# Kernel tuning notes

Measured on AMD Instinct MI355X. Metric: run time of the kernel, lower is better.

Reference implementation:

```python
import jax, jax.numpy as jnp
import numpy as np
import math

B, S, D, H, W = 1, 2048, 512, 8, 64
DK = D // H
NEG = -1e9


def setup_inputs() -> dict:
    rng = jax.random.key(0)
    ks = jax.random.split(rng, 8)
    sc = 0.02
    return {
        "query": jax.random.normal(ks[0], (B, S, D), jnp.float32),
        "key": jax.random.normal(ks[1], (B, S, D), jnp.float32),
        "value": jax.random.normal(ks[2], (B, S, D), jnp.float32),
        "Wq": jax.random.normal(ks[3], (D, D), jnp.float32) * sc,
        "Wk": jax.random.normal(ks[4], (D, D), jnp.float32) * sc,
        "Wv": jax.random.normal(ks[5], (D, D), jnp.float32) * sc,
        "Wo": jax.random.normal(ks[6], (D, D), jnp.float32) * sc,
        "bo": jax.random.normal(ks[7], (D,), jnp.float32) * sc,
    }


def reference(query, key, value, Wq, Wk, Wv, Wo, bo):
    b, s, d = query.shape

    def proj(x, Wm):
        # [B,S,D] -> [B,H,S,DK]
        return (x @ Wm.T).reshape(b, s, H, DK).transpose(0, 2, 1, 3)

    Q = proj(query, Wq)
    K = proj(key, Wk)
    V = proj(value, Wv)

    i = jnp.arange(s)
    rel = jnp.arange(-W, 1)                     # causal band: keys i-W..i
    idx = i[:, None] + rel[None, :]             # [S, W+1]
    valid = idx >= 0
    idxc = jnp.clip(idx, 0, s - 1)

    Kw = K[:, :, idxc, :]                       # [B,H,S,W+1,DK]
    Vw = V[:, :, idxc, :]

    scores = jnp.einsum('bhsd,bhsrd->bhsr', Q, Kw) / math.sqrt(DK)
    decay_bias = 0.1 * jnp.exp(-0.1 * jnp.abs(rel.astype(jnp.float32)))
    scores = jnp.where(valid[None, None], scores + decay_bias, NEG)
    probs = jax.nn.softmax(scores, axis=-1)     # [B,H,S,W+1]

    out = jnp.einsum('bhsr,bhsrd->bhsd', probs, Vw)
    out = out.transpose(0, 2, 1, 3).reshape(b, s, d)
    output = out @ Wo.T + bo

    # attention_weights [B,H,S,2W]: only rows with window_size <= 2W are written
    win = jnp.minimum(s, i + W + 1) - jnp.maximum(0, i - W)   # [S]
    stored = win <= 2 * W
    slot = jnp.arange(2 * W)
    ridx = slot[None, :] + jnp.maximum(W - i, 0)[:, None]     # [S,2W] slot->band index
    vmask = (ridx <= W) & (slot[None, :] < win[:, None]) & stored[:, None]
    gath = jnp.take_along_axis(probs, jnp.clip(ridx, 0, W)[None, None], axis=-1)
    attn_w = jnp.where(vmask[None, None], gath, 0.0)

    return output, attn_w
```

## Files before the change

kernel.cpp:

```cpp
#include <hip/hip_runtime.h>
#include <stdint.h>

#define SEQ   2048
#define DM    512
#define NHEAD 8
#define DKH   64
#define WIN   64
#define NEGV  -1000000000.0f

typedef __attribute__((ext_vector_type(8))) short          short8;
typedef __attribute__((ext_vector_type(4))) float          float4v;
typedef __attribute__((ext_vector_type(8))) unsigned short ushort8v;

__device__ __forceinline__ unsigned short f2bf(float x) {
    uint32_t u = __float_as_uint(x);
    uint32_t r = (u + 0x7FFFu + ((u >> 16) & 1u)) >> 16;
    return (unsigned short)r;
}
__device__ __forceinline__ float bf2f(unsigned short u) {
    return __uint_as_float(((uint32_t)u) << 16);
}

__device__ __forceinline__ void async_cp16(const void* g, void* lds) {
    __builtin_amdgcn_global_load_lds(
        (const __attribute__((address_space(1))) unsigned int*)(uintptr_t)g,
        (__attribute__((address_space(3))) unsigned int*)(uint32_t)(uintptr_t)lds,
        16, 0, 0);
}

__global__ __launch_bounds__(256)
void cast7_kernel(const float* __restrict__ q, const float* __restrict__ k,
                  const float* __restrict__ v, const float* __restrict__ wq,
                  const float* __restrict__ wk, const float* __restrict__ wv,
                  const float* __restrict__ wo, unsigned short* __restrict__ dst)
{
    int g = (blockIdx.x * 256 + threadIdx.x) * 8;
    const float* src; int off;
    if      (g < 1048576) { src = q;  off = g; }
    else if (g < 2097152) { src = k;  off = g - 1048576; }
    else if (g < 3145728) { src = v;  off = g - 2097152; }
    else if (g < 3407872) { src = wq; off = g - 3145728; }
    else if (g < 3670016) { src = wk; off = g - 3407872; }
    else if (g < 3932160) { src = wv; off = g - 3670016; }
    else                  { src = wo; off = g - 3932160; }
    float4 x0 = *(const float4*)(src + off);
    float4 x1 = *(const float4*)(src + off + 4);
    ushort8v o;
    o[0] = f2bf(x0.x); o[1] = f2bf(x0.y); o[2] = f2bf(x0.z); o[3] = f2bf(x0.w);
    o[4] = f2bf(x1.x); o[5] = f2bf(x1.y); o[6] = f2bf(x1.z); o[7] = f2bf(x1.w);
    *(ushort8v*)(dst + g) = o;
}

template<bool BIAS, bool OUT_BF16>
__device__ __forceinline__ void gemm_mfma_body(const unsigned short* __restrict__ A,
                                               const unsigned short* __restrict__ B,
                                               const float* __restrict__ bias,
                                               void* __restrict__ Cv)
{
    __shared__ __align__(16) unsigned short As[2][128 * 32];
    __shared__ __align__(16) unsigned short Bs[2][128 * 32];

    const int tid  = threadIdx.x;
    const int m0   = blockIdx.x * 128;
    const int n0   = blockIdx.y * 128;
    const int lane = tid & 63;
    const int wave = tid >> 6;
    const int wm   = (wave >> 1) * 64;
    const int wn   = (wave & 1) * 64;
    const int lm   = lane & 15;
    const int lk   = (lane >> 4) * 8;

    float4v acc[4][4] = {};

    #pragma unroll
    for (int h = 0; h < 2; h++) {
        int c  = tid + h * 256;
        int rr = c >> 2;
        int kk = (c & 3) * 8;
        async_cp16(A + (size_t)(m0 + rr) * 512 + kk, &As[0][c * 8]);
        async_cp16(B + (size_t)(n0 + rr) * 512 + kk, &Bs[0][c * 8]);
    }
    __syncthreads();

    for (int t = 0; t < 16; ++t) {
        const int cur = t & 1;
        if (t < 15) {
            const int k0 = (t + 1) * 32;
            #pragma unroll
            for (int h = 0; h < 2; h++) {
                int c  = tid + h * 256;
                int rr = c >> 2;
                int kk = (c & 3) * 8;
                async_cp16(A + (size_t)(m0 + rr) * 512 + k0 + kk, &As[cur ^ 1][c * 8]);
                async_cp16(B + (size_t)(n0 + rr) * 512 + k0 + kk, &Bs[cur ^ 1][c * 8]);
            }
        }

        short8 av[4], bv[4];
        #pragma unroll
        for (int mt = 0; mt < 4; mt++)
            av[mt] = *(const short8*)(&As[cur][(wm + mt * 16 + lm) * 32 + lk]);
        #pragma unroll
        for (int nt = 0; nt < 4; nt++)
            bv[nt] = *(const short8*)(&Bs[cur][(wn + nt * 16 + lm) * 32 + lk]);
        #pragma unroll
        for (int mt = 0; mt < 4; mt++)
            #pragma unroll
            for (int nt = 0; nt < 4; nt++)
                acc[mt][nt] = __builtin_amdgcn_mfma_f32_16x16x32_bf16(
                    av[mt], bv[nt], acc[mt][nt], 0, 0, 0);

        __syncthreads();
    }

    const int r0 = (lane >> 4) * 4;
    const int cn = lane & 15;
    #pragma unroll
    for (int nt = 0; nt < 4; nt++) {
        int gcol = n0 + wn + nt * 16 + cn;
        float b = BIAS ? bias[gcol] : 0.f;
        #pragma unroll
        for (int mt = 0; mt < 4; mt++) {
            int grow = m0 + wm + mt * 16 + r0;
            #pragma unroll
            for (int reg = 0; reg < 4; reg++) {
                float val = acc[mt][nt][reg] + b;
                if (OUT_BF16)
                    ((unsigned short*)Cv)[(size_t)(grow + reg) * 512 + gcol] = f2bf(val);
                else
                    ((float*)Cv)[(size_t)(grow + reg) * 512 + gcol] = val;
            }
        }
    }
}

__global__ __launch_bounds__(256)
void qkv_gemm_kernel(const unsigned short* __restrict__ qb,
                     const unsigned short* __restrict__ kb,
                     const unsigned short* __restrict__ vb,
                     const unsigned short* __restrict__ wqb,
                     const unsigned short* __restrict__ wkb,
                     const unsigned short* __restrict__ wvb,
                     unsigned short* __restrict__ Qp, unsigned short* __restrict__ Kp,
                     unsigned short* __restrict__ Vp)
{
    const unsigned short *A, *B; unsigned short* C;
    if (blockIdx.z == 0)      { A = qb; B = wqb; C = Qp; }
    else if (blockIdx.z == 1) { A = kb; B = wkb; C = Kp; }
    else                      { A = vb; B = wvb; C = Vp; }
    gemm_mfma_body<false, true>(A, B, nullptr, C);
}

__global__ __launch_bounds__(256)
void out_gemm_kernel(const unsigned short* __restrict__ ctxb,
                     const unsigned short* __restrict__ wob,
                     const float* __restrict__ bo, float* __restrict__ out)
{
    gemm_mfma_body<true, false>(ctxb, wob, bo, out);
}

#define VTS 152

__global__ __launch_bounds__(256)
void attn_kernel(const unsigned short* __restrict__ Qp,
                 const unsigned short* __restrict__ Kp,
                 const unsigned short* __restrict__ Vp,
                 unsigned short* __restrict__ ctxb,
                 float* __restrict__ attnw)
{
    __shared__ __align__(16) unsigned short Qs[64 * 72];
    __shared__ __align__(16) unsigned short Ks[128 * 72];
    __shared__ __align__(16) unsigned short Vt[64 * VTS];
    __shared__ __align__(16) unsigned short Ps[4][16][96];

    const int h   = blockIdx.y;
    const int q0  = blockIdx.x * 64;
    const int tid = threadIdx.x;

    for (int c = tid; c < 512; c += 256) {
        int row = c >> 3, ch = c & 7;
        *(ushort8v*)&Qs[row * 72 + ch * 8] =
            *(const ushort8v*)&Qp[(size_t)(q0 + row) * 512 + h * 64 + ch * 8];
    }
    for (int c = tid; c < 1024; c += 256) {
        int row = c >> 3, ch = c & 7;
        int g = q0 - 64 + row;
        ushort8v val = {0, 0, 0, 0, 0, 0, 0, 0};
        if (g >= 0)
            val = *(const ushort8v*)&Kp[(size_t)g * 512 + h * 64 + ch * 8];
        *(ushort8v*)&Ks[row * 72 + ch * 8] = val;
    }
    {
        int key = tid >> 1, dh = tid & 1;
        int g = q0 - 64 + key;
        ushort8v vv[4];
        #pragma unroll
        for (int j = 0; j < 4; j++) {
            ushort8v z = {0, 0, 0, 0, 0, 0, 0, 0};
            vv[j] = (g >= 0)
                ? *(const ushort8v*)&Vp[(size_t)g * 512 + h * 64 + dh * 32 + j * 8]
                : z;
        }
        #pragma unroll
        for (int j = 0; j < 4; j++)
            #pragma unroll
            for (int e = 0; e < 8; e++)
                Vt[(dh * 32 + j * 8 + e) * VTS + key] = vv[j][e];
    }
    for (int t = tid; t < 64 * 24; t += 256) {
        int d = t / 24, c = 128 + (t % 24);
        Vt[d * VTS + c] = 0;
    }
    __syncthreads();

    const int lane = tid & 63;
    const int w    = tid >> 6;
    const int lm   = lane & 15;
    const int g16  = lane >> 4;
    const int lk8  = g16 * 8;

    short8 av0 = *(const short8*)&Qs[(w * 16 + lm) * 72 + lk8];
    short8 av1 = *(const short8*)&Qs[(w * 16 + lm) * 72 + 32 + lk8];
    float4v sc[5];
    #pragma unroll
    for (int kt = 0; kt < 5; kt++) {
        const unsigned short* kr = &Ks[(w * 16 + kt * 16 + lm) * 72];
        short8 b0 = *(const short8*)(kr + lk8);
        short8 b1 = *(const short8*)(kr + 32 + lk8);
        float4v a = {0.f, 0.f, 0.f, 0.f};
        a = __builtin_amdgcn_mfma_f32_16x16x32_bf16(av0, b0, a, 0, 0, 0);
        a = __builtin_amdgcn_mfma_f32_16x16x32_bf16(av1, b1, a, 0, 0, 0);
        sc[kt] = a;
    }

    float v[5][4];
    #pragma unroll
    for (int kt = 0; kt < 5; kt++) {
        int kk = kt * 16 + lm;
        int g  = q0 - 64 + w * 16 + kk;
        #pragma unroll
        for (int reg = 0; reg < 4; reg++) {
            int rr = g16 * 4 + reg;
            bool valid = (kk >= rr) && (kk <= rr + 64) && (g >= 0);
            v[kt][reg] = valid
                ? sc[kt][reg] * 0.125f + 0.1f * __expf(-0.1f * (float)(64 + rr - kk))
                : NEGV;
        }
    }

    float mx[4], sm[4];
    #pragma unroll
    for (int reg = 0; reg < 4; reg++) {
        float m = v[0][reg];
        #pragma unroll
        for (int kt = 1; kt < 5; kt++) m = fmaxf(m, v[kt][reg]);
        mx[reg] = m;
    }
    #pragma unroll
    for (int off = 1; off < 16; off <<= 1)
        #pragma unroll
        for (int reg = 0; reg < 4; reg++)
            mx[reg] = fmaxf(mx[reg], __shfl_xor(mx[reg], off));
    float p[5][4];
    #pragma unroll
    for (int reg = 0; reg < 4; reg++) {
        float s = 0.f;
        #pragma unroll
        for (int kt = 0; kt < 5; kt++) {
            float e = __expf(v[kt][reg] - mx[reg]);
            p[kt][reg] = e;
            s += e;
        }
        sm[reg] = s;
    }
    #pragma unroll
    for (int off = 1; off < 16; off <<= 1)
        #pragma unroll
        for (int reg = 0; reg < 4; reg++)
            sm[reg] += __shfl_xor(sm[reg], off);
    #pragma unroll
    for (int reg = 0; reg < 4; reg++) {
        float inv = 1.f / sm[reg];
        #pragma unroll
        for (int kt = 0; kt < 5; kt++) p[kt][reg] *= inv;
    }

    #pragma unroll
    for (int kt = 0; kt < 5; kt++)
        #pragma unroll
        for (int reg = 0; reg < 4; reg++)
            Ps[w][g16 * 4 + reg][kt * 16 + lm] = f2bf(p[kt][reg]);
    #pragma unroll
    for (int reg = 0; reg < 4; reg++)
        Ps[w][g16 * 4 + reg][80 + lm] = 0;

    __syncthreads();

    float4v oacc[4] = {};
    #pragma unroll
    for (int ks = 0; ks < 3; ks++) {
        short8 pa = *(const short8*)&Ps[w][lm][ks * 32 + lk8];
        #pragma unroll
        for (int nt = 0; nt < 4; nt++) {
            short8 vb = *(const short8*)&Vt[(nt * 16 + lm) * VTS + w * 16 + ks * 32 + lk8];
            oacc[nt] = __builtin_amdgcn_mfma_f32_16x16x32_bf16(pa, vb, oacc[nt], 0, 0, 0);
        }
    }

    #pragma unroll
    for (int nt = 0; nt < 4; nt++)
        #pragma unroll
        for (int reg = 0; reg < 4; reg++) {
            int i = q0 + w * 16 + g16 * 4 + reg;
            ctxb[(size_t)i * 512 + h * 64 + nt * 16 + lm] = f2bf(oacc[nt][reg]);
        }

    __syncthreads();

    for (int t = tid; t < 64 * 128; t += 256) {
        int ql = t >> 7, slot = t & 127;
        int i  = q0 + ql;
        float val = 0.f;
        if (q0 == 0) {
            if (slot <= ql) {
                int kk = (ql & 15) + slot + 64 - ql;
                val = bf2f(Ps[ql >> 4][ql & 15][kk]);
            }
        } else if (q0 == SEQ - 64) {
            if (slot <= 64) {
                int kk = (ql & 15) + slot;
                val = bf2f(Ps[ql >> 4][ql & 15][kk]);
            }
        }
        attnw[((size_t)h * SEQ + i) * 2 * WIN + slot] = val;
    }
}

extern "C" void kernel_launch(void* const* d_in, const int* in_sizes, int n_in,
                              void* d_out, int out_size, void* d_ws, size_t ws_size,
                              hipStream_t stream)
{
    const float* query = (const float*)d_in[0];
    const float* key   = (const float*)d_in[1];
    const float* value = (const float*)d_in[2];
    const float* Wq    = (const float*)d_in[3];
    const float* Wk    = (const float*)d_in[4];
    const float* Wv    = (const float*)d_in[5];
    const float* Wo    = (const float*)d_in[6];
    const float* bo    = (const float*)d_in[7];

    float* out   = (float*)d_out;
    float* attnw = out + SEQ * DM;

    unsigned short* qb   = (unsigned short*)d_ws;
    unsigned short* kb   = qb  + 1048576;
    unsigned short* vb   = kb  + 1048576;
    unsigned short* wqb  = vb  + 1048576;
    unsigned short* wkb  = wqb + 262144;
    unsigned short* wvb  = wkb + 262144;
    unsigned short* wob  = wvb + 262144;
    unsigned short* Qp   = wob + 262144;
    unsigned short* Kp   = Qp  + 1048576;
    unsigned short* Vp   = Kp  + 1048576;
    unsigned short* ctxb = Vp  + 1048576;

    cast7_kernel<<<2048, 256, 0, stream>>>(query, key, value, Wq, Wk, Wv, Wo, qb);

    dim3 g1(SEQ / 128, DM / 128, 3);
    qkv_gemm_kernel<<<g1, 256, 0, stream>>>(qb, kb, vb, wqb, wkb, wvb, Qp, Kp, Vp);

    dim3 g2(SEQ / 64, NHEAD);
    attn_kernel<<<g2, 256, 0, stream>>>(Qp, Kp, Vp, ctxb, attnw);

    dim3 g3(SEQ / 128, DM / 128);
    out_gemm_kernel<<<g3, 256, 0, stream>>>(ctxb, wob, bo, out);
}
```

Baseline: 109.6 us.

## Fuse fp32-to-bf16 cast into GEMM loads and vectorize attention-weight stores

```diff
diff --git a/kernel.cpp b/kernel.cpp
--- a/kernel.cpp
+++ b/kernel.cpp
@@ -21,106 +21,131 @@
     return __uint_as_float(((uint32_t)u) << 16);
 }
 
-__device__ __forceinline__ void async_cp16(const void* g, void* lds) {
-    __builtin_amdgcn_global_load_lds(
-        (const __attribute__((address_space(1))) unsigned int*)(uintptr_t)g,
-        (__attribute__((address_space(3))) unsigned int*)(uint32_t)(uintptr_t)lds,
-        16, 0, 0);
-}
-
-__global__ __launch_bounds__(256)
-void cast7_kernel(const float* __restrict__ q, const float* __restrict__ k,
-                  const float* __restrict__ v, const float* __restrict__ wq,
-                  const float* __restrict__ wk, const float* __restrict__ wv,
-                  const float* __restrict__ wo, unsigned short* __restrict__ dst)
+template<bool A_F32, bool B_F32, bool BIAS, bool OUT_BF16, int BM, int BN>
+__device__ __forceinline__ void gemm_body(const void* __restrict__ Ap,
+                                          const void* __restrict__ Bp,
+                                          const float* __restrict__ bias,
+                                          void* __restrict__ Cv)
 {
-    int g = (blockIdx.x * 256 + threadIdx.x) * 8;
-    const float* src; int off;
-    if      (g < 1048576) { src = q;  off = g; }
-    else if (g < 2097152) { src = k;  off = g - 1048576; }
-    else if (g < 3145728) { src = v;  off = g - 2097152; }
-    else if (g < 3407872) { src = wq; off = g - 3145728; }
-    else if (g < 3670016) { src = wk; off = g - 3407872; }
-    else if (g < 3932160) { src = wv; off = g - 3670016; }
-    else                  { src = wo; off = g - 3932160; }
-    float4 x0 = *(const float4*)(src + off);
-    float4 x1 = *(const float4*)(src + off + 4);
-    ushort8v o;
-    o[0] = f2bf(x0.x); o[1] = f2bf(x0.y); o[2] = f2bf(x0.z); o[3] = f2bf(x0.w);
-    o[4] = f2bf(x1.x); o[5] = f2bf(x1.y); o[6] = f2bf(x1.z); o[7] = f2bf(x1.w);
-    *(ushort8v*)(dst + g) = o;
-}
-
-template<bool BIAS, bool OUT_BF16>
-__device__ __forceinline__ void gemm_mfma_body(const unsigned short* __restrict__ A,
-                                               const unsigned short* __restrict__ B,
-                                               const float* __restrict__ bias,
-                                               void* __restrict__ Cv)
-{
-    __shared__ __align__(16) unsigned short As[2][128 * 32];
-    __shared__ __align__(16) unsigned short Bs[2][128 * 32];
+    __shared__ __align__(16) unsigned short As[2][BM * 32];
+    __shared__ __align__(16) unsigned short Bs[2][BN * 32];
+
+    constexpr int HA = BM / 64;
+    constexpr int HB = BN / 64;
+    constexpr int FM = BM / 32;
+    constexpr int FN = BN / 32;
 
     const int tid  = threadIdx.x;
-    const int m0   = blockIdx.x * 128;
-    const int n0   = blockIdx.y * 128;
+    const int m0   = blockIdx.x * BM;
+    const int n0   = blockIdx.y * BN;
     const int lane = tid & 63;
     const int wave = tid >> 6;
-    const int wm   = (wave >> 1) * 64;
-    const int wn   = (wave & 1) * 64;
+    const int wm   = (wave >> 1) * (BM / 2);
+    const int wn   = (wave & 1) * (BN / 2);
     const int lm   = lane & 15;
     const int lk   = (lane >> 4) * 8;
 
-    float4v acc[4][4] = {};
-
-    #pragma unroll
-    for (int h = 0; h < 2; h++) {
-        int c  = tid + h * 256;
-        int rr = c >> 2;
-        int kk = (c & 3) * 8;
-        async_cp16(A + (size_t)(m0 + rr) * 512 + kk, &As[0][c * 8]);
-        async_cp16(B + (size_t)(n0 + rr) * 512 + kk, &Bs[0][c * 8]);
-    }
+    float4v acc[FM][FN] = {};
+
+    float4   raf[HA][2]; ushort8v rab[HA];
+    float4   rbf[HB][2]; ushort8v rbb[HB];
+
+    auto load_regs = [&](int k0) {
+        #pragma unroll
+        for (int h = 0; h < HA; h++) {
+            int c = tid + h * 256;
+            int r = c >> 2, kc = (c & 3) * 8;
+            if constexpr (A_F32) {
+                const float* p = (const float*)Ap + (size_t)(m0 + r) * 512 + k0 + kc;
+                raf[h][0] = *(const float4*)p;
+                raf[h][1] = *(const float4*)(p + 4);
+            } else {
+                rab[h] = *(const ushort8v*)((const unsigned short*)Ap +
+                                            (size_t)(m0 + r) * 512 + k0 + kc);
+            }
+        }
+        #pragma unroll
+        for (int h = 0; h < HB; h++) {
+            int c = tid + h * 256;
+            int r = c >> 2, kc = (c & 3) * 8;
+            if constexpr (B_F32) {
+                const float* p = (const float*)Bp + (size_t)(n0 + r) * 512 + k0 + kc;
+                rbf[h][0] = *(const float4*)p;
+                rbf[h][1] = *(const float4*)(p + 4);
+            } else {
+                rbb[h] = *(const ushort8v*)((const unsigned short*)Bp +
+                                            (size_t)(n0 + r) * 512 + k0 + kc);
+            }
+        }
+    };
+    auto store_lds = [&](int buf) {
+        #pragma unroll
+        for (int h = 0; h < HA; h++) {
+            int c = tid + h * 256;
+            int r = c >> 2, kc = (c & 3) * 8;
+            ushort8v o;
+            if constexpr (A_F32) {
+                o[0] = f2bf(raf[h][0].x); o[1] = f2bf(raf[h][0].y);
+                o[2] = f2bf(raf[h][0].z); o[3] = f2bf(raf[h][0].w);
+                o[4] = f2bf(raf[h][1].x); o[5] = f2bf(raf[h][1].y);
+                o[6] = f2bf(raf[h][1].z); o[7] = f2bf(raf[h][1].w);
+            } else {
+                o = rab[h];
+            }
+            *(ushort8v*)&As[buf][r * 32 + kc] = o;
+        }
+        #pragma unroll
+        for (int h = 0; h < HB; h++) {
+            int c = tid + h * 256;
+            int r = c >> 2, kc = (c & 3) * 8;
+            ushort8v o;
+            if constexpr (B_F32) {
+                o[0] = f2bf(rbf[h][0].x); o[1] = f2bf(rbf[h][0].y);
+                o[2] = f2bf(rbf[h][0].z); o[3] = f2bf(rbf[h][0].w);
+                o[4] = f2bf(rbf[h][1].x); o[5] = f2bf(rbf[h][1].y);
+                o[6] = f2bf(rbf[h][1].z); o[7] = f2bf(rbf[h][1].w);
+            } else {
+                o = rbb[h];
+            }
+            *(ushort8v*)&Bs[buf][r * 32 + kc] = o;
+        }
+    };
+
+    load_regs(0);
+    store_lds(0);
+    load_regs(32);
     __syncthreads();
 
     for (int t = 0; t < 16; ++t) {
         const int cur = t & 1;
-        if (t < 15) {
-            const int k0 = (t + 1) * 32;
+        short8 av[FM], bv[FN];
+        #pragma unroll
+        for (int mt = 0; mt < FM; mt++)
+            av[mt] = *(const short8*)&As[cur][(wm + mt * 16 + lm) * 32 + lk];
+        #pragma unroll
+        for (int nt = 0; nt < FN; nt++)
+            bv[nt] = *(const short8*)&Bs[cur][(wn + nt * 16 + lm) * 32 + lk];
+        #pragma unroll
+        for (int mt = 0; mt < FM; mt++)
             #pragma unroll
-            for (int h = 0; h < 2; h++) {
-                int c  = tid + h * 256;
-                int rr = c >> 2;
-                int kk = (c & 3) * 8;
-                async_cp16(A + (size_t)(m0 + rr) * 512 + k0 + kk, &As[cur ^ 1][c * 8]);
-                async_cp16(B + (size_t)(n0 + rr) * 512 + k0 + kk, &Bs[cur ^ 1][c * 8]);
-            }
-        }
-
-        short8 av[4], bv[4];
-        #pragma unroll
-        for (int mt = 0; mt < 4; mt++)
-            av[mt] = *(const short8*)(&As[cur][(wm + mt * 16 + lm) * 32 + lk]);
-        #pragma unroll
-        for (int nt = 0; nt < 4; nt++)
-            bv[nt] = *(const short8*)(&Bs[cur][(wn + nt * 16 + lm) * 32 + lk]);
-        #pragma unroll
-        for (int mt = 0; mt < 4; mt++)
-            #pragma unroll
-            for (int nt = 0; nt < 4; nt++)
+            for (int nt = 0; nt < FN; nt++)
                 acc[mt][nt] = __builtin_amdgcn_mfma_f32_16x16x32_bf16(
                     av[mt], bv[nt], acc[mt][nt], 0, 0, 0);
-
+        if (t < 15) {
+            store_lds(cur ^ 1);
+            if (t < 14) load_regs((t + 2) * 32);
+        }
         __syncthreads();
     }
 
     const int r0 = (lane >> 4) * 4;
     const int cn = lane & 15;
     #pragma unroll
-    for (int nt = 0; nt < 4; nt++) {
+    for (int nt = 0; nt < FN; nt++) {
         int gcol = n0 + wn + nt * 16 + cn;
         float b = BIAS ? bias[gcol] : 0.f;
         #pragma unroll
-        for (int mt = 0; mt < 4; mt++) {
+        for (int mt = 0; mt < FM; mt++) {
             int grow = m0 + wm + mt * 16 + r0;
             #pragma unroll
             for (int reg = 0; reg < 4; reg++) {
@@ -135,28 +160,25 @@
 }
 
 __global__ __launch_bounds__(256)
-void qkv_gemm_kernel(const unsigned short* __restrict__ qb,
-                     const unsigned short* __restrict__ kb,
-                     const unsigned short* __restrict__ vb,
-                     const unsigned short* __restrict__ wqb,
-                     const unsigned short* __restrict__ wkb,
-                     const unsigned short* __restrict__ wvb,
+void qkv_gemm_kernel(const float* __restrict__ q, const float* __restrict__ k,
+                     const float* __restrict__ v, const float* __restrict__ wq,
+                     const float* __restrict__ wk, const float* __restrict__ wv,
                      unsigned short* __restrict__ Qp, unsigned short* __restrict__ Kp,
                      unsigned short* __restrict__ Vp)
 {
-    const unsigned short *A, *B; unsigned short* C;
-    if (blockIdx.z == 0)      { A = qb; B = wqb; C = Qp; }
-    else if (blockIdx.z == 1) { A = kb; B = wkb; C = Kp; }
-    else                      { A = vb; B = wvb; C = Vp; }
-    gemm_mfma_body<false, true>(A, B, nullptr, C);
+    const float *A, *B; unsigned short* C;
+    if (blockIdx.z == 0)      { A = q; B = wq; C = Qp; }
+    else if (blockIdx.z == 1) { A = k; B = wk; C = Kp; }
+    else                      { A = v; B = wv; C = Vp; }
+    gemm_body<true, true, false, true, 128, 128>(A, B, nullptr, C);
 }
 
 __global__ __launch_bounds__(256)
 void out_gemm_kernel(const unsigned short* __restrict__ ctxb,
-                     const unsigned short* __restrict__ wob,
+                     const float* __restrict__ wo,
                      const float* __restrict__ bo, float* __restrict__ out)
 {
-    gemm_mfma_body<true, false>(ctxb, wob, bo, out);
+    gemm_body<false, true, true, false, 128, 64>(ctxb, wo, bo, out);
 }
 
 #define VTS 152
@@ -317,22 +339,35 @@
 
     __syncthreads();
 
-    for (int t = tid; t < 64 * 128; t += 256) {
-        int ql = t >> 7, slot = t & 127;
+    for (int t = tid; t < 1024; t += 256) {
+        int ql = t >> 4;
+        int s0 = (t & 15) * 8;
         int i  = q0 + ql;
-        float val = 0.f;
+        float4 v0 = {0.f, 0.f, 0.f, 0.f}, v1 = {0.f, 0.f, 0.f, 0.f};
         if (q0 == 0) {
-            if (slot <= ql) {
-                int kk = (ql & 15) + slot + 64 - ql;
-                val = bf2f(Ps[ql >> 4][ql & 15][kk]);
+            #pragma unroll
+            for (int e = 0; e < 8; e++) {
+                int slot = s0 + e;
+                if (slot <= ql) {
+                    int kk = (ql & 15) + slot + 64 - ql;
+                    float vv = bf2f(Ps[ql >> 4][ql & 15][kk]);
+                    if (e < 4) ((float*)&v0)[e] = vv; else ((float*)&v1)[e - 4] = vv;
+                }
             }
         } else if (q0 == SEQ - 64) {
-            if (slot <= 64) {
-                int kk = (ql & 15) + slot;
-                val = bf2f(Ps[ql >> 4][ql & 15][kk]);
-            }
-        }
-        attnw[((size_t)h * SEQ + i) * 2 * WIN + slot] = val;
+            #pragma unroll
+            for (int e = 0; e < 8; e++) {
+                int slot = s0 + e;
+                if (slot <= 64) {
+                    int kk = (ql & 15) + slot;
+                    float vv = bf2f(Ps[ql >> 4][ql & 15][kk]);
+                    if (e < 4) ((float*)&v0)[e] = vv; else ((float*)&v1)[e - 4] = vv;
+                }
+            }
+        }
+        float* dst = &attnw[((size_t)h * SEQ + i) * 2 * WIN + s0];
+        *(float4*)dst       = v0;
+        *(float4*)(dst + 4) = v1;
     }
 }
 
@@ -352,26 +387,17 @@
     float* out   = (float*)d_out;
     float* attnw = out + SEQ * DM;
 
-    unsigned short* qb   = (unsigned short*)d_ws;
-    unsigned short* kb   = qb  + 1048576;
-    unsigned short* vb   = kb  + 1048576;
-    unsigned short* wqb  = vb  + 1048576;
-    unsigned short* wkb  = wqb + 262144;
-    unsigned short* wvb  = wkb + 262144;
-    unsigned short* wob  = wvb + 262144;
-    unsigned short* Qp   = wob + 262144;
-    unsigned short* Kp   = Qp  + 1048576;
-    unsigned short* Vp   = Kp  + 1048576;
-    unsigned short* ctxb = Vp  + 1048576;
-
-    cast7_kernel<<<2048, 256, 0, stream>>>(query, key, value, Wq, Wk, Wv, Wo, qb);
+    unsigned short* Qp   = (unsigned short*)d_ws;
+    unsigned short* Kp   = Qp + 1048576;
+    unsigned short* Vp   = Kp + 1048576;
+    unsigned short* ctxb = Vp + 1048576;
 
     dim3 g1(SEQ / 128, DM / 128, 3);
-    qkv_gemm_kernel<<<g1, 256, 0, stream>>>(qb, kb, vb, wqb, wkb, wvb, Qp, Kp, Vp);
+    qkv_gemm_kernel<<<g1, 256, 0, stream>>>(query, key, value, Wq, Wk, Wv, Qp, Kp, Vp);
 
     dim3 g2(SEQ / 64, NHEAD);
     attn_kernel<<<g2, 256, 0, stream>>>(Qp, Kp, Vp, ctxb, attnw);
 
-    dim3 g3(SEQ / 128, DM / 128);
-    out_gemm_kernel<<<g3, 256, 0, stream>>>(ctxb, wob, bo, out);
-}
+    dim3 g3(SEQ / 128, DM / 64);
+    out_gemm_kernel<<<g3, 256, 0, stream>>>(ctxb, Wo, bo, out);
+}
```

After: 108.2 us. No clear change (-1.3%).
